# Performance work log

Hardware: AMD Instinct MI355X
Metric: run time of the kernel (lower is better)

Reference implementation:

```python
import jax, jax.numpy as jnp
import numpy as np

N_EMBD = 1024
NUM_HEADS = 16
HEAD_DIM = N_EMBD // NUM_HEADS
B, N = 4, 1024
EPS = 1e-5


def _ln(x, w, b):
    mu = jnp.mean(x, axis=-1, keepdims=True)
    var = jnp.var(x, axis=-1, keepdims=True)
    return (x - mu) * jax.lax.rsqrt(var + EPS) * w + b


def setup_inputs() -> dict:
    key = jax.random.key(0)
    ks = jax.random.split(key, 12)
    s = 0.02
    d, dff = N_EMBD, 4 * N_EMBD
    return {
        "x": jax.random.normal(ks[0], (B, N, d), dtype=jnp.float32),
        "ln1_w": jnp.ones((d,), jnp.float32),
        "ln1_b": jnp.zeros((d,), jnp.float32),
        "Wq": jax.random.normal(ks[1], (d, d), jnp.float32) * s,
        "bq": jnp.zeros((d,), jnp.float32),
        "Wk": jax.random.normal(ks[2], (d, d), jnp.float32) * s,
        "bk": jnp.zeros((d,), jnp.float32),
        "Wv": jax.random.normal(ks[3], (d, d), jnp.float32) * s,
        "bv": jnp.zeros((d,), jnp.float32),
        "Wo": jax.random.normal(ks[4], (d, d), jnp.float32) * s,
        "bo": jnp.zeros((d,), jnp.float32),
        "ln2_w": jnp.ones((d,), jnp.float32),
        "ln2_b": jnp.zeros((d,), jnp.float32),
        "Wfc": jax.random.normal(ks[5], (d, dff), jnp.float32) * s,
        "bfc": jnp.zeros((dff,), jnp.float32),
        "Wproj": jax.random.normal(ks[6], (dff, d), jnp.float32) * s,
        "bproj": jnp.zeros((d,), jnp.float32),
    }


def reference(x, ln1_w, ln1_b, Wq, bq, Wk, bk, Wv, bv, Wo, bo,
              ln2_w, ln2_b, Wfc, bfc, Wproj, bproj):
    # --- attention sublayer ---
    h = _ln(x, ln1_w, ln1_b)  # [B,N,D]
    q = (h @ Wq + bq).reshape(B, N, NUM_HEADS, HEAD_DIM).transpose(0, 2, 1, 3)
    k = (h @ Wk + bk).reshape(B, N, NUM_HEADS, HEAD_DIM).transpose(0, 2, 1, 3)
    v = (h @ Wv + bv).reshape(B, N, NUM_HEADS, HEAD_DIM).transpose(0, 2, 1, 3)
    scale = 1.0 / np.sqrt(HEAD_DIM).astype(np.float32)
    attn = jax.nn.softmax(jnp.einsum("bhqd,bhkd->bhqk", q, k) * scale, axis=-1)
    o = jnp.einsum("bhqk,bhkd->bhqd", attn, v)  # [B,H,N,Dh]
    o = o.transpose(0, 2, 1, 3).reshape(B, N, N_EMBD)
    x = x + (o @ Wo + bo)
    # --- MLP sublayer (exact GELU, matching torch nn.GELU default) ---
    h2 = _ln(x, ln2_w, ln2_b)
    h2 = jax.nn.gelu(h2 @ Wfc + bfc, approximate=False)
    x = x + (h2 @ Wproj + bproj)
    return x
```

## Files before the change

kernel.cpp:

```cpp
#include <hip/hip_runtime.h>
#include <hip/hip_bf16.h>

typedef unsigned short u16;
typedef u16 u16x8 __attribute__((ext_vector_type(8)));
typedef u16 u16x4 __attribute__((ext_vector_type(4)));
typedef __bf16 bf16x8 __attribute__((ext_vector_type(8)));
typedef float f32x4 __attribute__((ext_vector_type(4)));

__device__ __forceinline__ u16 f2bf(float f) {
  union { __hip_bfloat16 h; u16 u; } cv;
  cv.h = __float2bfloat16(f);
  return cv.u;
}
__device__ __forceinline__ float bf2f(u16 u) {
  union { unsigned u; float f; } c;
  c.u = ((unsigned)u) << 16;
  return c.f;
}

__device__ __forceinline__ void glds16(const void* g, void* l) {
  __builtin_amdgcn_global_load_lds(
      (const __attribute__((address_space(1))) unsigned int*)g,
      (__attribute__((address_space(3))) unsigned int*)l, 16, 0, 0);
}

__global__ __launch_bounds__(256) void transpose_bf16(const float* __restrict__ W,
                                                      u16* __restrict__ Wt,
                                                      int K, int N) {
  __shared__ float tile[32][33];
  int tx = threadIdx.x, ty = threadIdx.y;
  int n0 = blockIdx.x * 32, k0 = blockIdx.y * 32;
#pragma unroll
  for (int j = 0; j < 4; ++j)
    tile[ty + j * 8][tx] = W[(size_t)(k0 + ty + j * 8) * N + n0 + tx];
  __syncthreads();
#pragma unroll
  for (int j = 0; j < 4; ++j)
    Wt[(size_t)(n0 + ty + j * 8) * K + k0 + tx] = f2bf(tile[tx][ty + j * 8]);
}

__global__ __launch_bounds__(256) void transpose4(const float* __restrict__ W0,
                                                  const float* __restrict__ W1,
                                                  const float* __restrict__ W2,
                                                  const float* __restrict__ W3,
                                                  u16* __restrict__ T0, u16* __restrict__ T1,
                                                  u16* __restrict__ T2, u16* __restrict__ T3) {
  __shared__ float tile[32][33];
  int z = blockIdx.z;
  const float* W = (z == 0) ? W0 : (z == 1) ? W1 : (z == 2) ? W2 : W3;
  u16* T = (z == 0) ? T0 : (z == 1) ? T1 : (z == 2) ? T2 : T3;
  int tx = threadIdx.x, ty = threadIdx.y;
  int n0 = blockIdx.x * 32, k0 = blockIdx.y * 32;
#pragma unroll
  for (int j = 0; j < 4; ++j)
    tile[ty + j * 8][tx] = W[(size_t)(k0 + ty + j * 8) * 1024 + n0 + tx];
  __syncthreads();
#pragma unroll
  for (int j = 0; j < 4; ++j)
    T[(size_t)(n0 + ty + j * 8) * 1024 + k0 + tx] = f2bf(tile[tx][ty + j * 8]);
}

__global__ __launch_bounds__(256) void ln_kernel(const float* __restrict__ x,
                                                 const float* __restrict__ w,
                                                 const float* __restrict__ b,
                                                 u16* __restrict__ out) {
  int row = blockIdx.x, t = threadIdx.x;
  const float* xr = x + (size_t)row * 1024;
  float4 v = *reinterpret_cast<const float4*>(xr + t * 4);
  float s = v.x + v.y + v.z + v.w;
  float s2 = v.x * v.x + v.y * v.y + v.z * v.z + v.w * v.w;
#pragma unroll
  for (int m = 1; m < 64; m <<= 1) {
    s += __shfl_xor(s, m, 64);
    s2 += __shfl_xor(s2, m, 64);
  }
  __shared__ float red[8];
  if ((t & 63) == 0) { red[t >> 6] = s; red[(t >> 6) + 4] = s2; }
  __syncthreads();
  s = red[0] + red[1] + red[2] + red[3];
  s2 = red[4] + red[5] + red[6] + red[7];
  float mu = s * (1.f / 1024.f);
  float var = s2 * (1.f / 1024.f) - mu * mu;
  float rs = rsqrtf(var + 1e-5f);
  float4 wv = *reinterpret_cast<const float4*>(w + t * 4);
  float4 bv = *reinterpret_cast<const float4*>(b + t * 4);
  u16x4 o;
  o.x = f2bf((v.x - mu) * rs * wv.x + bv.x);
  o.y = f2bf((v.y - mu) * rs * wv.y + bv.y);
  o.z = f2bf((v.z - mu) * rs * wv.z + bv.z);
  o.w = f2bf((v.w - mu) * rs * wv.w + bv.w);
  *reinterpret_cast<u16x4*>(out + (size_t)row * 1024 + t * 4) = o;
}

template <int MODE>
__global__ __launch_bounds__(512, 2) void gemm256(
    const u16* __restrict__ A, const u16* __restrict__ Bt,
    const float* __restrict__ b0, const float* __restrict__ b1,
    const float* __restrict__ b2,
    u16* __restrict__ o0, u16* __restrict__ o1, u16* __restrict__ o2,
    u16* __restrict__ o3,
    int Kfull, int KL, int MT, int NT, float qscale) {
  __shared__ u16 lds[2][2][2][256 * 32];
  const int tid = threadIdx.x;
  const int lane = tid & 63, w = tid >> 6;
  const int wm = w >> 2, wn = w & 3;
  const int l15 = lane & 15, l4 = lane >> 4;
  const int skey = (l15 >> 1) & 3;

  const int nwg = gridDim.x;
  int wg = (int)blockIdx.x;
  wg = (wg & 7) * (nwg >> 3) + (wg >> 3);
  const int mt = wg % MT;
  int rest = wg / MT;
  const int nt = rest % NT;
  const int zt = rest / NT;

  const int row0 = mt * 256, col0 = nt * 256;
  const int kbase = zt * KL;
  const int nkt = KL >> 6;

  auto stage = [&](int buf, int op, int ks, int kt) {
    const u16* src = op ? Bt : A;
    const int base = op ? col0 : row0;
    const int kb = kbase + (kt << 6) + (ks << 5);
    u16* dst = &lds[buf][op][ks][0];
#pragma unroll
    for (int i = 0; i < 2; ++i) {
      int c = i * 512 + tid;
      int r = c >> 2, ch = c & 3;
      int sch = ch ^ ((r >> 1) & 3);
      glds16(src + (size_t)(base + r) * Kfull + kb + sch * 8, dst + c * 8);
    }
  };
  auto rdA = [&](int buf, int ks, int m) -> bf16x8 {
    int row = wm * 128 + m * 16 + l15;
    return *reinterpret_cast<const bf16x8*>(&lds[buf][0][ks][row * 32 + ((l4 ^ skey) << 3)]);
  };
  auto rdB = [&](int buf, int ks, int n) -> bf16x8 {
    int row = wn * 64 + n * 16 + l15;
    return *reinterpret_cast<const bf16x8*>(&lds[buf][1][ks][row * 32 + ((l4 ^ skey) << 3)]);
  };

  f32x4 acc[8][4];
#pragma unroll
  for (int m = 0; m < 8; ++m)
#pragma unroll
    for (int n = 0; n < 4; ++n) acc[m][n] = (f32x4){0.f, 0.f, 0.f, 0.f};

  stage(0, 0, 0, 0);
  stage(0, 0, 1, 0);
  stage(0, 1, 0, 0);
  stage(0, 1, 1, 0);
  asm volatile("s_waitcnt vmcnt(2)" ::: "memory");
  __builtin_amdgcn_s_barrier();

  bf16x8 af[8];
  for (int t = 0; t < nkt; ++t) {
    const int cur = t & 1, nxt = cur ^ 1;
    const bool pf = (t + 1 < nkt);
    {
#pragma unroll
      for (int m = 0; m < 8; ++m) af[m] = rdA(cur, 0, m);
      bf16x8 bq0 = rdB(cur, 0, 0), bq1 = rdB(cur, 0, 1);
      if (pf) stage(nxt, 0, 0, t + 1);
      __builtin_amdgcn_s_barrier();
      __builtin_amdgcn_s_setprio(1);
#pragma unroll
      for (int m = 0; m < 8; ++m) {
        acc[m][0] = __builtin_amdgcn_mfma_f32_16x16x32_bf16(af[m], bq0, acc[m][0], 0, 0, 0);
        acc[m][1] = __builtin_amdgcn_mfma_f32_16x16x32_bf16(af[m], bq1, acc[m][1], 0, 0, 0);
      }
      __builtin_amdgcn_s_setprio(0);
      __builtin_amdgcn_s_barrier();
    }
    {
      bf16x8 bq2 = rdB(cur, 0, 2), bq3 = rdB(cur, 0, 3);
      if (pf) {
        stage(nxt, 0, 1, t + 1);
        asm volatile("s_waitcnt vmcnt(4)" ::: "memory");
      } else {
        asm volatile("s_waitcnt vmcnt(0)" ::: "memory");
      }
      __builtin_amdgcn_s_barrier();
      __builtin_amdgcn_s_setprio(1);
#pragma unroll
      for (int m = 0; m < 8; ++m) {
        acc[m][2] = __builtin_amdgcn_mfma_f32_16x16x32_bf16(af[m], bq2, acc[m][2], 0, 0, 0);
        acc[m][3] = __builtin_amdgcn_mfma_f32_16x16x32_bf16(af[m], bq3, acc[m][3], 0, 0, 0);
      }
      __builtin_amdgcn_s_setprio(0);
      __builtin_amdgcn_s_barrier();
    }
    {
#pragma unroll
      for (int m = 0; m < 8; ++m) af[m] = rdA(cur, 1, m);
      bf16x8 bq0 = rdB(cur, 1, 0), bq1 = rdB(cur, 1, 1);
      if (pf) stage(nxt, 1, 0, t + 1);
      __builtin_amdgcn_s_barrier();
      __builtin_amdgcn_s_setprio(1);
#pragma unroll
      for (int m = 0; m < 8; ++m) {
        acc[m][0] = __builtin_amdgcn_mfma_f32_16x16x32_bf16(af[m], bq0, acc[m][0], 0, 0, 0);
        acc[m][1] = __builtin_amdgcn_mfma_f32_16x16x32_bf16(af[m], bq1, acc[m][1], 0, 0, 0);
      }
      __builtin_amdgcn_s_setprio(0);
      __builtin_amdgcn_s_barrier();
    }
    {
      bf16x8 bq2 = rdB(cur, 1, 2), bq3 = rdB(cur, 1, 3);
      if (pf) stage(nxt, 1, 1, t + 1);
      asm volatile("s_waitcnt vmcnt(2)" ::: "memory");
      __builtin_amdgcn_s_barrier();
      __builtin_amdgcn_s_setprio(1);
#pragma unroll
      for (int m = 0; m < 8; ++m) {
        acc[m][2] = __builtin_amdgcn_mfma_f32_16x16x32_bf16(af[m], bq2, acc[m][2], 0, 0, 0);
        acc[m][3] = __builtin_amdgcn_mfma_f32_16x16x32_bf16(af[m], bq3, acc[m][3], 0, 0, 0);
      }
      __builtin_amdgcn_s_setprio(0);
      __builtin_amdgcn_s_barrier();
    }
  }

  if constexpr (MODE == 0) {
    const int which = nt >> 2;
    const int bidx = mt >> 2;
#pragma unroll
    for (int m = 0; m < 8; ++m)
#pragma unroll
      for (int n = 0; n < 4; ++n) {
        int colc = (col0 & 1023) + wn * 64 + n * 16 + l15;
        int hh = colc >> 6, d = colc & 63;
        int nb = (row0 & 1023) + wm * 128 + m * 16 + l4 * 4;
        if (which == 2) {
          u16x4 pk;
#pragma unroll
          for (int r = 0; r < 4; ++r) pk[r] = f2bf(acc[m][n][r] + b2[colc]);
          *reinterpret_cast<u16x4*>(o2 + (((size_t)(bidx * 16 + hh) * 64 + d) * 1024 + nb)) = pk;
        } else {
          const float* bb = (which == 0) ? b0 : b1;
          u16* dst = (which == 0) ? o0 : o1;
          float sc = (which == 0) ? qscale : 1.0f;
#pragma unroll
          for (int r = 0; r < 4; ++r)
            dst[((size_t)(bidx * 16 + hh) * 1024 + nb + r) * 64 + d] =
                f2bf((acc[m][n][r] + bb[colc]) * sc);
        }
      }
  } else if constexpr (MODE == 2) {
    const int N = NT * 256;
#pragma unroll
    for (int m = 0; m < 8; ++m)
#pragma unroll
      for (int n = 0; n < 4; ++n)
#pragma unroll
        for (int r = 0; r < 4; ++r) {
          int row = row0 + wm * 128 + m * 16 + l4 * 4 + r;
          int col = col0 + wn * 64 + n * 16 + l15;
          float val = acc[m][n][r] + b0[col];
          float g = 0.5f * val * (1.0f + erff(val * 0.70710678118f));
          o0[(size_t)row * N + col] = f2bf(g);
        }
  } else {
    const int N = NT * 256;
    u16* base = (zt == 0) ? o0 : (zt == 1) ? o1 : (zt == 2) ? o2 : o3;
#pragma unroll
    for (int m = 0; m < 8; ++m)
#pragma unroll
      for (int n = 0; n < 4; ++n)
#pragma unroll
        for (int r = 0; r < 4; ++r) {
          int row = row0 + wm * 128 + m * 16 + l4 * 4 + r;
          int col = col0 + wn * 64 + n * 16 + l15;
          base[(size_t)row * N + col] = f2bf(acc[m][n][r]);
        }
  }
}

__global__ __launch_bounds__(256) void reduce4(const u16* __restrict__ p0,
                                               const u16* __restrict__ p1,
                                               const u16* __restrict__ p2,
                                               const u16* __restrict__ p3,
                                               const float* __restrict__ bias,
                                               const float* __restrict__ res,
                                               float* __restrict__ out) {
  size_t i = ((size_t)blockIdx.x * 256 + threadIdx.x) * 8;
  int col = (int)(i & 1023);
  float s[8];
  float4 r0 = *reinterpret_cast<const float4*>(res + i);
  float4 r1 = *reinterpret_cast<const float4*>(res + i + 4);
  s[0] = r0.x; s[1] = r0.y; s[2] = r0.z; s[3] = r0.w;
  s[4] = r1.x; s[5] = r1.y; s[6] = r1.z; s[7] = r1.w;
#pragma unroll
  for (int j = 0; j < 8; ++j) s[j] += bias[col + j];
  const u16* ps[4] = {p0, p1, p2, p3};
#pragma unroll
  for (int sp = 0; sp < 4; ++sp) {
    u16x8 pv = *reinterpret_cast<const u16x8*>(ps[sp] + i);
#pragma unroll
    for (int j = 0; j < 8; ++j) s[j] += bf2f(pv[j]);
  }
  float4 o0 = {s[0], s[1], s[2], s[3]};
  float4 o1 = {s[4], s[5], s[6], s[7]};
  *reinterpret_cast<float4*>(out + i) = o0;
  *reinterpret_cast<float4*>(out + i + 4) = o1;
}

__global__ __launch_bounds__(256) void attn_kernel(const u16* __restrict__ q,
                                                   const u16* __restrict__ k,
                                                   const u16* __restrict__ vt,
                                                   u16* __restrict__ o) {
  const int bh = blockIdx.x, qb = blockIdx.y;
  const int b = bh >> 4, h = bh & 15;
  __shared__ u16 Ks[2][4096];
  __shared__ u16 Vt[2][4096];
  __shared__ u16 Ps[4][1024];
  const int tid = threadIdx.x, lane = tid & 63, w = tid >> 6;
  const int l15 = lane & 15, l4 = lane >> 4;
  const int sw = l15 & 7;
  const u16* kbase = k + (size_t)bh * 65536;
  const u16* vtbase = vt + (size_t)bh * 65536;

  const u16* qrow = q + ((size_t)bh * 1024 + qb * 64 + w * 16 + l15) * 64;
  bf16x8 qf0 = *reinterpret_cast<const bf16x8*>(qrow + l4 * 8);
  bf16x8 qf1 = *reinterpret_cast<const bf16x8*>(qrow + 32 + l4 * 8);

  auto stageKV = [&](int buf, int kv0) {
#pragma unroll
    for (int i = 0; i < 2; ++i) {
      int c = i * 256 + tid, r = c >> 3, sl = (c & 7) ^ (r & 7);
      glds16(kbase + (size_t)(kv0 + r) * 64 + sl * 8, &Ks[buf][c * 8]);
    }
#pragma unroll
    for (int i = 0; i < 2; ++i) {
      int c = i * 256 + tid, r = c >> 3, sl = (c & 7) ^ (r & 7);
      glds16(vtbase + (size_t)r * 1024 + kv0 + sl * 8, &Vt[buf][c * 8]);
    }
  };

  f32x4 oacc[4];
#pragma unroll
  for (int n = 0; n < 4; ++n) oacc[n] = (f32x4){0.f, 0.f, 0.f, 0.f};
  float mrow = -3.0e38f, lrow = 0.f;

  stageKV(0, 0);
  __syncthreads();

  for (int kv0 = 0; kv0 < 1024; kv0 += 64) {
    int cur = (kv0 >> 6) & 1;
    if (kv0 + 64 < 1024) stageKV(cur ^ 1, kv0 + 64);

    f32x4 st[4];
#pragma unroll
    for (int t = 0; t < 4; ++t) {
      int row = t * 16 + l15;
      f32x4 s = (f32x4){0.f, 0.f, 0.f, 0.f};
      bf16x8 kf0 = *reinterpret_cast<const bf16x8*>(&Ks[cur][row * 64 + ((l4 ^ sw) << 3)]);
      s = __builtin_amdgcn_mfma_f32_16x16x32_bf16(kf0, qf0, s, 0, 0, 0);
      bf16x8 kf1 = *reinterpret_cast<const bf16x8*>(&Ks[cur][row * 64 + (((4 + l4) ^ sw) << 3)]);
      s = __builtin_amdgcn_mfma_f32_16x16x32_bf16(kf1, qf1, s, 0, 0, 0);
      st[t] = s;
    }

    float tm = st[0][0];
#pragma unroll
    for (int t = 0; t < 4; ++t)
#pragma unroll
      for (int r = 0; r < 4; ++r) tm = fmaxf(tm, st[t][r]);
    tm = fmaxf(tm, __shfl_xor(tm, 16, 64));
    tm = fmaxf(tm, __shfl_xor(tm, 32, 64));
    if (!__all(tm - mrow <= 8.f)) {
      float mnew = fmaxf(mrow, tm);
      float al = exp2f(mrow - mnew);
      lrow *= al;
#pragma unroll
      for (int n = 0; n < 4; ++n)
#pragma unroll
        for (int r = 0; r < 4; ++r) oacc[n][r] *= al;
      mrow = mnew;
    }
    float pr[4][4];
    float ps = 0.f;
#pragma unroll
    for (int t = 0; t < 4; ++t)
#pragma unroll
      for (int r = 0; r < 4; ++r) {
        pr[t][r] = exp2f(st[t][r] - mrow);
        ps += pr[t][r];
      }
    ps += __shfl_xor(ps, 16, 64);
    ps += __shfl_xor(ps, 32, 64);
    lrow += ps;

#pragma unroll
    for (int t = 0; t < 4; ++t) {
      u16x4 pk;
#pragma unroll
      for (int r = 0; r < 4; ++r) pk[r] = f2bf(pr[t][r]);
      int swch = ((t << 1) | (l4 >> 1)) ^ sw;
      *reinterpret_cast<u16x4*>(&Ps[w][l15 * 64 + swch * 8 + (l4 & 1) * 4]) = pk;
    }

#pragma unroll
    for (int c2 = 0; c2 < 2; ++c2) {
      bf16x8 pf = *reinterpret_cast<const bf16x8*>(
          &Ps[w][l15 * 64 + ((((c2 << 2) | l4) ^ sw) << 3)]);
#pragma unroll
      for (int n = 0; n < 4; ++n) {
        bf16x8 vf = *reinterpret_cast<const bf16x8*>(
            &Vt[cur][(n * 16 + l15) * 64 + ((((c2 << 2) | l4) ^ sw) << 3)]);
        oacc[n] = __builtin_amdgcn_mfma_f32_16x16x32_bf16(vf, pf, oacc[n], 0, 0, 0);
      }
    }
    __syncthreads();
  }

  float inv = 1.0f / lrow;
  int nr = qb * 64 + w * 16 + l15;
#pragma unroll
  for (int n = 0; n < 4; ++n) {
    u16x4 pk;
#pragma unroll
    for (int r = 0; r < 4; ++r) pk[r] = f2bf(oacc[n][r] * inv);
    *reinterpret_cast<u16x4*>(
        o + ((size_t)(b * 1024 + nr)) * 1024 + h * 64 + n * 16 + l4 * 4) = pk;
  }
}

extern "C" void kernel_launch(void* const* d_in, const int* in_sizes, int n_in,
                              void* d_out, int out_size, void* d_ws, size_t ws_size,
                              hipStream_t stream) {
  (void)in_sizes; (void)n_in; (void)out_size; (void)ws_size;
  const float* x     = (const float*)d_in[0];
  const float* ln1w  = (const float*)d_in[1];
  const float* ln1b  = (const float*)d_in[2];
  const float* Wq    = (const float*)d_in[3];
  const float* bq    = (const float*)d_in[4];
  const float* Wk    = (const float*)d_in[5];
  const float* bk    = (const float*)d_in[6];
  const float* Wv    = (const float*)d_in[7];
  const float* bv    = (const float*)d_in[8];
  const float* Wo    = (const float*)d_in[9];
  const float* bo    = (const float*)d_in[10];
  const float* ln2w  = (const float*)d_in[11];
  const float* ln2b  = (const float*)d_in[12];
  const float* Wfc   = (const float*)d_in[13];
  const float* bfc   = (const float*)d_in[14];
  const float* Wproj = (const float*)d_in[15];
  const float* bproj = (const float*)d_in[16];
  float* out = (float*)d_out;

  char* p = (char*)d_ws;
  u16* hb     = (u16*)p; p += (size_t)4096 * 1024 * 2;
  u16* WqkvT  = (u16*)p; p += (size_t)3072 * 1024 * 2;
  u16* WoT    = (u16*)p; p += (size_t)1024 * 1024 * 2;
  u16* WfcT   = (u16*)p; p += (size_t)4096 * 1024 * 2;
  u16* WprojT = (u16*)p; p += (size_t)1024 * 4096 * 2;
  u16* qb_    = (u16*)p; p += (size_t)4096 * 1024 * 2;
  u16* kb_    = (u16*)p; p += (size_t)4096 * 1024 * 2;
  u16* vt_    = (u16*)p; p += (size_t)4096 * 1024 * 2;
  u16* ob_    = (u16*)p; p += (size_t)4096 * 1024 * 2;
  float* x1   = (float*)p; p += (size_t)4096 * 1024 * 4;
  u16* h2     = (u16*)p; p += (size_t)4096 * 1024 * 2;
  u16* ffnb   = (u16*)p; p += (size_t)4096 * 4096 * 2;

  const float qscale = 0.125f * 1.44269504089f;

  dim3 tb(32, 8);
  transpose4<<<dim3(32, 32, 4), tb, 0, stream>>>(Wq, Wk, Wv, Wo,
                                                 WqkvT, WqkvT + (size_t)1024 * 1024,
                                                 WqkvT + (size_t)2048 * 1024, WoT);
  transpose_bf16<<<dim3(128, 32), tb, 0, stream>>>(Wfc, WfcT, 1024, 4096);
  transpose_bf16<<<dim3(32, 128), tb, 0, stream>>>(Wproj, WprojT, 4096, 1024);

  ln_kernel<<<4096, 256, 0, stream>>>(x, ln1w, ln1b, hb);

  gemm256<0><<<192, 512, 0, stream>>>(hb, WqkvT, bq, bk, bv,
                                      qb_, kb_, vt_, nullptr, 1024, 1024, 16, 12, qscale);

  attn_kernel<<<dim3(64, 16), 256, 0, stream>>>(qb_, kb_, vt_, ob_);

  gemm256<3><<<256, 512, 0, stream>>>(ob_, WoT, nullptr, nullptr, nullptr,
                                      qb_, kb_, vt_, h2, 1024, 256, 16, 4, 1.f);
  reduce4<<<2048, 256, 0, stream>>>(qb_, kb_, vt_, h2, bo, x, x1);

  ln_kernel<<<4096, 256, 0, stream>>>(x1, ln2w, ln2b, h2);

  gemm256<2><<<256, 512, 0, stream>>>(h2, WfcT, bfc, nullptr, nullptr,
                                      ffnb, nullptr, nullptr, nullptr, 1024, 1024, 16, 16, 1.f);

  gemm256<3><<<256, 512, 0, stream>>>(ffnb, WprojT, nullptr, nullptr, nullptr,
                                      qb_, kb_, vt_, ob_, 4096, 1024, 16, 4, 1.f);
  reduce4<<<2048, 256, 0, stream>>>(qb_, kb_, vt_, ob_, bproj, x1, out);
}
```

Baseline: 358.8 us.

## Reblock GEMM inner loop as 4x4 MFMA tiles and drop trailing barriers

```diff
diff --git a/kernel.cpp b/kernel.cpp
--- a/kernel.cpp
+++ b/kernel.cpp
@@ -119,17 +119,19 @@
   const int kbase = zt * KL;
   const int nkt = KL >> 6;
 
-  auto stage = [&](int buf, int op, int ks, int kt) {
-    const u16* src = op ? Bt : A;
-    const int base = op ? col0 : row0;
+  auto stageAB = [&](int buf, int ks, int kt) {
     const int kb = kbase + (kt << 6) + (ks << 5);
-    u16* dst = &lds[buf][op][ks][0];
 #pragma unroll
     for (int i = 0; i < 2; ++i) {
       int c = i * 512 + tid;
-      int r = c >> 2, ch = c & 3;
-      int sch = ch ^ ((r >> 1) & 3);
-      glds16(src + (size_t)(base + r) * Kfull + kb + sch * 8, dst + c * 8);
+      int r = c >> 2, sch = (c & 3) ^ ((r >> 1) & 3);
+      glds16(A + (size_t)(row0 + r) * Kfull + kb + sch * 8, &lds[buf][0][ks][0] + c * 8);
+    }
+#pragma unroll
+    for (int i = 0; i < 2; ++i) {
+      int c = i * 512 + tid;
+      int r = c >> 2, sch = (c & 3) ^ ((r >> 1) & 3);
+      glds16(Bt + (size_t)(col0 + r) * Kfull + kb + sch * 8, &lds[buf][1][ks][0] + c * 8);
     }
   };
   auto rdA = [&](int buf, int ks, int m) -> bf16x8 {
@@ -147,36 +149,34 @@
 #pragma unroll
     for (int n = 0; n < 4; ++n) acc[m][n] = (f32x4){0.f, 0.f, 0.f, 0.f};
 
-  stage(0, 0, 0, 0);
-  stage(0, 0, 1, 0);
-  stage(0, 1, 0, 0);
-  stage(0, 1, 1, 0);
-  asm volatile("s_waitcnt vmcnt(2)" ::: "memory");
+  stageAB(0, 0, 0);
+  stageAB(0, 1, 0);
+  asm volatile("s_waitcnt vmcnt(4)" ::: "memory");
   __builtin_amdgcn_s_barrier();
 
-  bf16x8 af[8];
+  bf16x8 am[4], bn[4];
   for (int t = 0; t < nkt; ++t) {
     const int cur = t & 1, nxt = cur ^ 1;
     const bool pf = (t + 1 < nkt);
     {
 #pragma unroll
-      for (int m = 0; m < 8; ++m) af[m] = rdA(cur, 0, m);
-      bf16x8 bq0 = rdB(cur, 0, 0), bq1 = rdB(cur, 0, 1);
-      if (pf) stage(nxt, 0, 0, t + 1);
+      for (int m = 0; m < 4; ++m) am[m] = rdA(cur, 0, m);
+#pragma unroll
+      for (int n = 0; n < 4; ++n) bn[n] = rdB(cur, 0, n);
+      if (pf) stageAB(nxt, 0, t + 1);
       __builtin_amdgcn_s_barrier();
       __builtin_amdgcn_s_setprio(1);
 #pragma unroll
-      for (int m = 0; m < 8; ++m) {
-        acc[m][0] = __builtin_amdgcn_mfma_f32_16x16x32_bf16(af[m], bq0, acc[m][0], 0, 0, 0);
-        acc[m][1] = __builtin_amdgcn_mfma_f32_16x16x32_bf16(af[m], bq1, acc[m][1], 0, 0, 0);
-      }
+      for (int m = 0; m < 4; ++m)
+#pragma unroll
+        for (int n = 0; n < 4; ++n)
+          acc[m][n] = __builtin_amdgcn_mfma_f32_16x16x32_bf16(am[m], bn[n], acc[m][n], 0, 0, 0);
       __builtin_amdgcn_s_setprio(0);
-      __builtin_amdgcn_s_barrier();
     }
     {
-      bf16x8 bq2 = rdB(cur, 0, 2), bq3 = rdB(cur, 0, 3);
+#pragma unroll
+      for (int m = 0; m < 4; ++m) am[m] = rdA(cur, 0, m + 4);
       if (pf) {
-        stage(nxt, 0, 1, t + 1);
         asm volatile("s_waitcnt vmcnt(4)" ::: "memory");
       } else {
         asm volatile("s_waitcnt vmcnt(0)" ::: "memory");
@@ -184,41 +184,39 @@
       __builtin_amdgcn_s_barrier();
       __builtin_amdgcn_s_setprio(1);
 #pragma unroll
-      for (int m = 0; m < 8; ++m) {
-        acc[m][2] = __builtin_amdgcn_mfma_f32_16x16x32_bf16(af[m], bq2, acc[m][2], 0, 0, 0);
-        acc[m][3] = __builtin_amdgcn_mfma_f32_16x16x32_bf16(af[m], bq3, acc[m][3], 0, 0, 0);
-      }
+      for (int m = 0; m < 4; ++m)
+#pragma unroll
+        for (int n = 0; n < 4; ++n)
+          acc[m + 4][n] = __builtin_amdgcn_mfma_f32_16x16x32_bf16(am[m], bn[n], acc[m + 4][n], 0, 0, 0);
       __builtin_amdgcn_s_setprio(0);
-      __builtin_amdgcn_s_barrier();
     }
     {
 #pragma unroll
-      for (int m = 0; m < 8; ++m) af[m] = rdA(cur, 1, m);
-      bf16x8 bq0 = rdB(cur, 1, 0), bq1 = rdB(cur, 1, 1);
-      if (pf) stage(nxt, 1, 0, t + 1);
+      for (int m = 0; m < 4; ++m) am[m] = rdA(cur, 1, m);
+#pragma unroll
+      for (int n = 0; n < 4; ++n) bn[n] = rdB(cur, 1, n);
+      if (pf) stageAB(nxt, 1, t + 1);
       __builtin_amdgcn_s_barrier();
       __builtin_amdgcn_s_setprio(1);
 #pragma unroll
-      for (int m = 0; m < 8; ++m) {
-        acc[m][0] = __builtin_amdgcn_mfma_f32_16x16x32_bf16(af[m], bq0, acc[m][0], 0, 0, 0);
-        acc[m][1] = __builtin_amdgcn_mfma_f32_16x16x32_bf16(af[m], bq1, acc[m][1], 0, 0, 0);
-      }
+      for (int m = 0; m < 4; ++m)
+#pragma unroll
+        for (int n = 0; n < 4; ++n)
+          acc[m][n] = __builtin_amdgcn_mfma_f32_16x16x32_bf16(am[m], bn[n], acc[m][n], 0, 0, 0);
       __builtin_amdgcn_s_setprio(0);
-      __builtin_amdgcn_s_barrier();
     }
     {
-      bf16x8 bq2 = rdB(cur, 1, 2), bq3 = rdB(cur, 1, 3);
-      if (pf) stage(nxt, 1, 1, t + 1);
-      asm volatile("s_waitcnt vmcnt(2)" ::: "memory");
+#pragma unroll
+      for (int m = 0; m < 4; ++m) am[m] = rdA(cur, 1, m + 4);
+      asm volatile("s_waitcnt vmcnt(4)" ::: "memory");
       __builtin_amdgcn_s_barrier();
       __builtin_amdgcn_s_setprio(1);
 #pragma unroll
-      for (int m = 0; m < 8; ++m) {
-        acc[m][2] = __builtin_amdgcn_mfma_f32_16x16x32_bf16(af[m], bq2, acc[m][2], 0, 0, 0);
-        acc[m][3] = __builtin_amdgcn_mfma_f32_16x16x32_bf16(af[m], bq3, acc[m][3], 0, 0, 0);
-      }
+      for (int m = 0; m < 4; ++m)
+#pragma unroll
+        for (int n = 0; n < 4; ++n)
+          acc[m + 4][n] = __builtin_amdgcn_mfma_f32_16x16x32_bf16(am[m], bn[n], acc[m + 4][n], 0, 0, 0);
       __builtin_amdgcn_s_setprio(0);
-      __builtin_amdgcn_s_barrier();
     }
   }
 
```

New measurement: 362.0 us. Within noise of the previous version (+0.9%).
